# Optimization experiments

Hardware: AMD Instinct MI355X
Metric: run time of the kernel (lower is better)

## Reference

```python
import jax, jax.numpy as jnp
import numpy as np

PS = 2      # patch_size
TOPK = 3    # topk


def setup_inputs() -> dict:
    key = jax.random.key(0)
    x = jax.random.normal(key, (8, 128, 64, 64), dtype=jnp.float32)
    alpha = jnp.asarray(5.0, dtype=jnp.float32)  # nn.Parameter alpha
    return {"x": x, "alpha": alpha}


def _forward(x, alpha):
    ps = PS
    b, c, h, w = x.shape
    nph, npw = h // ps, w // ps
    npatch = nph * npw
    pa = ps * ps
    # F.normalize(p=2, dim=-3) with torch eps=1e-12
    norm = jnp.maximum(jnp.sqrt(jnp.sum(x * x, axis=1, keepdims=True)), 1e-12)
    x = x / norm
    # patchify -> [b, c, npatch, patch_area] (patches h-major, pixels row-major)
    xp = x.reshape(b, c, nph, ps, npw, ps).transpose(0, 1, 2, 4, 3, 5)
    xp = xp.reshape(b, c, npatch, pa)
    diag_idx = jnp.arange(ps) * (ps + 1)  # [0, 3] for ps=2
    # gather diagonal pixels of each patch -> [b, ps, npatch, c]
    xd = xp[:, :, :, diag_idx].transpose(0, 3, 2, 1)
    # patch correlation matmul -> [b, ps, npatch, npatch]
    corr = jnp.einsum('bpnc,bpmc->bpnm', xd, xd)
    avg = jnp.mean(corr, axis=1, keepdims=True)
    s = jnp.concatenate([corr, avg], axis=1)  # [b, ps+1, npatch, npatch]
    # ZeroWindow gaussian mask (rat_s=0.05); channel index = patch center (r,c)
    sr, sc = 0.05 * nph, 0.05 * npw
    rr = jnp.arange(nph, dtype=jnp.float32)
    cc = jnp.arange(npw, dtype=jnp.float32)
    cent_r, cent_c = jnp.meshgrid(rr, cc, indexing='ij')
    cent_r = cent_r.reshape(npatch)
    cent_c = cent_c.reshape(npatch)
    gr = jnp.exp(-(rr[None, :] - cent_r[:, None]) ** 2 / (2.0 * sr * sr))  # [npatch, nph]
    gc = jnp.exp(-(cc[None, :] - cent_c[:, None]) ** 2 / (2.0 * sc * sc))  # [npatch, npw]
    mask = (1.0 - gr[:, :, None] * gc[:, None, :]).reshape(npatch, npatch)
    s = s * mask[None, None]
    a = s * alpha
    # double (row + col) softmax
    s = jax.nn.softmax(a, axis=-1) * jax.nn.softmax(a, axis=-2)
    # expand avg channel to all patch pixels, scatter diagonal channels back
    new_x = jnp.broadcast_to(s[:, -1:], (b, pa, npatch, npatch))
    new_x = new_x.at[:, diag_idx].set(s[:, :ps])
    # un-patchify second npatch axis to spatial [b, npatch, h, w]
    y = jnp.swapaxes(new_x, 1, 3)  # [b, npatch, npatch, pa]
    y = y.reshape(b, npatch, nph, npw, ps, ps).transpose(0, 1, 2, 4, 3, 5)
    y = y.reshape(b, npatch, h, w)
    # topk over the npatch axis (dim=-3)
    vals = jax.lax.top_k(jnp.moveaxis(y, 1, -1), TOPK)[0]  # [b, h, w, k]
    return jnp.moveaxis(vals, -1, 1)  # [b, k, h, w]


def reference(x, alpha):
    return _forward(x, alpha)
```

## Files before the change

kernel.cpp:

```cpp
#include <hip/hip_runtime.h>
#include <hip/hip_bf16.h>
#include <math.h>

#define NB 8
#define NC 128
#define NH 64
#define NW 64
#define NP 1024
#define TWO_SIG2 5.12f

static const size_t RSUM_OFF_B = 0;
static const size_t PBUF_OFF_B = (size_t)NB * 3 * NP * 4;
static const size_t XD_OFF_B   = PBUF_OFF_B + (size_t)NB * NP * 3 * 4 * 3 * 4;

typedef __bf16 bf16x8 __attribute__((ext_vector_type(8)));
typedef float f32x4 __attribute__((ext_vector_type(4)));

__device__ __forceinline__ int iabs_(int v) { return v < 0 ? -v : v; }

#define INSERT3(v, A, Bq, Cq)                \
  {                                          \
    const float _c1 = fminf(A, (v));         \
    A = fmaxf(A, (v));                       \
    const float _c2 = fminf(Bq, _c1);        \
    Bq = fmaxf(Bq, _c1);                     \
    Cq = fmaxf(Cq, _c2);                     \
  }

#define MERGE3(a0, a1, a2, b0, b1, b2)       \
  {                                          \
    const float _x1 = fmaxf(a0, b0);         \
    const float _y1 = fminf(a0, b0);         \
    const float _x2 = fmaxf(a1, b1);         \
    const float _z  = fmaxf(a2, b2);         \
    a0 = _x1;                                \
    a1 = fmaxf(_y1, _x2);                    \
    a2 = fmaxf(fminf(_y1, _x2), _z);         \
  }

__global__ __launch_bounds__(256) void k1_norm(const float* __restrict__ x,
                                               __hip_bfloat16* __restrict__ xd) {
  __shared__ __align__(16) float tile[NC * 65];
  const int chunk = blockIdx.x;
  const int p = blockIdx.y;
  const int b = blockIdx.z;
  const int t = threadIdx.x;
  const int pix = t & 63;
  const int cw = t >> 6;
  const int nbase = chunk * 64;

  {
    const int n = nbase + pix;
    const int i = ((n >> 5) << 1) + p;
    const int j = ((n & 31) << 1) + p;
    const float* xb = x + (size_t)b * NC * NH * NW + (size_t)i * NW + j;
    for (int cc = 0; cc < 32; ++cc) {
      const int c = (cc << 2) + cw;
      tile[c * 65 + pix] = xb[(size_t)c * NH * NW];
    }
  }
  __syncthreads();

  const int lane = t & 63;
  const int w = t >> 6;
  for (int pg = 0; pg < 16; ++pg) {
    const int pixel = (pg << 2) + w;
    const float v0 = tile[lane * 65 + pixel];
    const float v1 = tile[(lane + 64) * 65 + pixel];
    float ss = v0 * v0 + v1 * v1;
#pragma unroll
    for (int m = 32; m >= 1; m >>= 1) ss += __shfl_xor(ss, m, 64);
    const float inv = 1.0f / fmaxf(sqrtf(ss), 1e-12f);
    __hip_bfloat16* xr = xd + ((size_t)((b * 2 + p) * NP) + nbase + pixel) * NC;
    xr[lane] = __float2bfloat16(v0 * inv);
    xr[lane + 64] = __float2bfloat16(v1 * inv);
  }
}

__global__ __launch_bounds__(256) void k2_sums(const ushort* __restrict__ xd,
                                               const float* __restrict__ alpha_p,
                                               float* __restrict__ rsum) {
  __shared__ __align__(16) __bf16 As[2][64 * 136];
  __shared__ __align__(16) __bf16 Bs[2][64 * 136];
  __shared__ float er[32];
  const int t = threadIdx.x;
  if (t < 32) er[t] = __expf(-(float)(t * t) / TWO_SIG2);

  const int cchunk = blockIdx.x;
  const int rowtile = blockIdx.y;
  const int b = blockIdx.z;
  const int i0 = rowtile << 6;
  const int jb = cchunk << 8;
  const float alpha = *alpha_p;

#pragma unroll
  for (int pl = 0; pl < 2; ++pl) {
    const float4* ga = (const float4*)(xd + ((size_t)(b * 2 + pl) * NP + i0) * NC);
#pragma unroll
    for (int it = 0; it < 4; ++it) {
      const int f = (it << 8) + t;
      const int r = f >> 4, q = f & 15;
      *(float4*)(&As[pl][r * 136 + q * 8]) = ga[f];
    }
  }

  const int wave = t >> 6;
  const int lane = t & 63;
  const int lrow = lane & 15;
  const int kq = lane >> 4;

  float sums[3][4];
#pragma unroll
  for (int ch = 0; ch < 3; ++ch)
#pragma unroll
    for (int reg = 0; reg < 4; ++reg) sums[ch][reg] = 0.f;

  for (int sc = 0; sc < 4; ++sc) {
    const int j0 = jb + (sc << 6);
    __syncthreads();
#pragma unroll
    for (int pl = 0; pl < 2; ++pl) {
      const float4* gb = (const float4*)(xd + ((size_t)(b * 2 + pl) * NP + j0) * NC);
#pragma unroll
      for (int it = 0; it < 4; ++it) {
        const int f = (it << 8) + t;
        const int r = f >> 4, q = f & 15;
        *(float4*)(&Bs[pl][r * 136 + q * 8]) = gb[f];
      }
    }
    __syncthreads();

    f32x4 acc[2][4];
#pragma unroll
    for (int pl = 0; pl < 2; ++pl)
#pragma unroll
      for (int ct = 0; ct < 4; ++ct)
#pragma unroll
        for (int u = 0; u < 4; ++u) acc[pl][ct][u] = 0.f;

#pragma unroll
    for (int kc = 0; kc < 4; ++kc) {
      const int kk = kc * 32 + (kq << 3);
      const bf16x8 a0 = *(const bf16x8*)(&As[0][(wave * 16 + lrow) * 136 + kk]);
      const bf16x8 a1 = *(const bf16x8*)(&As[1][(wave * 16 + lrow) * 136 + kk]);
#pragma unroll
      for (int ct = 0; ct < 4; ++ct) {
        const bf16x8 b0 = *(const bf16x8*)(&Bs[0][(ct * 16 + lrow) * 136 + kk]);
        const bf16x8 b1 = *(const bf16x8*)(&Bs[1][(ct * 16 + lrow) * 136 + kk]);
        acc[0][ct] = __builtin_amdgcn_mfma_f32_16x16x32_bf16(a0, b0, acc[0][ct], 0, 0, 0);
        acc[1][ct] = __builtin_amdgcn_mfma_f32_16x16x32_bf16(a1, b1, acc[1][ct], 0, 0, 0);
      }
    }

#pragma unroll
    for (int ct = 0; ct < 4; ++ct) {
      const int m = j0 + ct * 16 + lrow;
      const int rm = m >> 5, cm = m & 31;
#pragma unroll
      for (int reg = 0; reg < 4; ++reg) {
        const int n = i0 + wave * 16 + kq * 4 + reg;
        const int rn = n >> 5, cn = n & 31;
        const float g = er[iabs_(rn - rm)] * er[iabs_(cn - cm)];
        const float fm = alpha * (1.f - g);
        const float c0 = acc[0][ct][reg];
        const float c1 = acc[1][ct][reg];
        sums[0][reg] += __expf(fm * c0);
        sums[1][reg] += __expf(fm * c1);
        sums[2][reg] += __expf(fm * 0.5f * (c0 + c1));
      }
    }
  }

#pragma unroll
  for (int off = 1; off < 16; off <<= 1)
#pragma unroll
    for (int ch = 0; ch < 3; ++ch)
#pragma unroll
      for (int reg = 0; reg < 4; ++reg)
        sums[ch][reg] += __shfl_xor(sums[ch][reg], off, 64);

  if (lrow == 0) {
#pragma unroll
    for (int ch = 0; ch < 3; ++ch)
#pragma unroll
      for (int reg = 0; reg < 4; ++reg) {
        const int n = i0 + wave * 16 + kq * 4 + reg;
        atomicAdd(&rsum[((size_t)b * 3 + ch) * NP + n], sums[ch][reg]);
      }
  }
}

__global__ __launch_bounds__(256) void k4_topk(const ushort* __restrict__ xd,
                                               const float* __restrict__ alpha_p,
                                               const float* __restrict__ rsum,
                                               float* __restrict__ pbuf) {
  __shared__ __align__(16) __bf16 As[2][64 * 136];
  __shared__ __align__(16) __bf16 Bs[2][64 * 136];
  __shared__ float er[32];
  __shared__ float rsr[3][64];
  __shared__ float rsc[3][256];
  const int t = threadIdx.x;
  if (t < 32) er[t] = __expf(-(float)(t * t) / TWO_SIG2);

  const int cchunk = blockIdx.x;
  const int rowtile = blockIdx.y;
  const int b = blockIdx.z;
  const int i0 = rowtile << 6;
  const int jb = cchunk << 8;
  const float alpha = *alpha_p;

  if (t < 192) {
    const int ch = t >> 6, r = t & 63;
    rsr[ch][r] = 1.0f / rsum[((size_t)b * 3 + ch) * NP + i0 + r];
  }
#pragma unroll
  for (int ch = 0; ch < 3; ++ch)
    rsc[ch][t] = 1.0f / rsum[((size_t)b * 3 + ch) * NP + jb + t];

#pragma unroll
  for (int pl = 0; pl < 2; ++pl) {
    const float4* ga = (const float4*)(xd + ((size_t)(b * 2 + pl) * NP + i0) * NC);
#pragma unroll
    for (int it = 0; it < 4; ++it) {
      const int f = (it << 8) + t;
      const int r = f >> 4, q = f & 15;
      *(float4*)(&As[pl][r * 136 + q * 8]) = ga[f];
    }
  }

  const int wave = t >> 6;
  const int lane = t & 63;
  const int lrow = lane & 15;
  const int kq = lane >> 4;

  float tA[3][4], tB[3][4], tC[3][4];
#pragma unroll
  for (int ch = 0; ch < 3; ++ch)
#pragma unroll
    for (int reg = 0; reg < 4; ++reg) { tA[ch][reg] = -1e30f; tB[ch][reg] = -1e30f; tC[ch][reg] = -1e30f; }

  for (int sc = 0; sc < 4; ++sc) {
    const int j0 = jb + (sc << 6);
    __syncthreads();
#pragma unroll
    for (int pl = 0; pl < 2; ++pl) {
      const float4* gb = (const float4*)(xd + ((size_t)(b * 2 + pl) * NP + j0) * NC);
#pragma unroll
      for (int it = 0; it < 4; ++it) {
        const int f = (it << 8) + t;
        const int r = f >> 4, q = f & 15;
        *(float4*)(&Bs[pl][r * 136 + q * 8]) = gb[f];
      }
    }
    __syncthreads();

    f32x4 acc[2][4];
#pragma unroll
    for (int pl = 0; pl < 2; ++pl)
#pragma unroll
      for (int ct = 0; ct < 4; ++ct)
#pragma unroll
        for (int u = 0; u < 4; ++u) acc[pl][ct][u] = 0.f;

#pragma unroll
    for (int kc = 0; kc < 4; ++kc) {
      const int kk = kc * 32 + (kq << 3);
      const bf16x8 a0 = *(const bf16x8*)(&As[0][(wave * 16 + lrow) * 136 + kk]);
      const bf16x8 a1 = *(const bf16x8*)(&As[1][(wave * 16 + lrow) * 136 + kk]);
#pragma unroll
      for (int ct = 0; ct < 4; ++ct) {
        const bf16x8 b0 = *(const bf16x8*)(&Bs[0][(ct * 16 + lrow) * 136 + kk]);
        const bf16x8 b1 = *(const bf16x8*)(&Bs[1][(ct * 16 + lrow) * 136 + kk]);
        acc[0][ct] = __builtin_amdgcn_mfma_f32_16x16x32_bf16(a0, b0, acc[0][ct], 0, 0, 0);
        acc[1][ct] = __builtin_amdgcn_mfma_f32_16x16x32_bf16(a1, b1, acc[1][ct], 0, 0, 0);
      }
    }

#pragma unroll
    for (int ct = 0; ct < 4; ++ct) {
      const int mc = sc * 64 + ct * 16 + lrow;
      const int m = jb + mc;
      const int rm = m >> 5, cm = m & 31;
      const float im0 = rsc[0][mc], im1 = rsc[1][mc], im2 = rsc[2][mc];
#pragma unroll
      for (int reg = 0; reg < 4; ++reg) {
        const int nr = wave * 16 + kq * 4 + reg;
        const int n = i0 + nr;
        const int rn = n >> 5, cn = n & 31;
        const float g = er[iabs_(rn - rm)] * er[iabs_(cn - cm)];
        const float fm = alpha * (1.f - g);
        const float c0 = acc[0][ct][reg];
        const float c1 = acc[1][ct][reg];
        const float e0 = __expf(fm * c0);
        const float e1 = __expf(fm * c1);
        const float e2 = __expf(fm * 0.5f * (c0 + c1));
        const float q0 = e0 * e0 * rsr[0][nr] * im0;
        const float q1 = e1 * e1 * rsr[1][nr] * im1;
        const float q2 = e2 * e2 * rsr[2][nr] * im2;
        INSERT3(q0, tA[0][reg], tB[0][reg], tC[0][reg]);
        INSERT3(q1, tA[1][reg], tB[1][reg], tC[1][reg]);
        INSERT3(q2, tA[2][reg], tB[2][reg], tC[2][reg]);
      }
    }
  }

#pragma unroll
  for (int off = 1; off < 16; off <<= 1)
#pragma unroll
    for (int ch = 0; ch < 3; ++ch)
#pragma unroll
      for (int reg = 0; reg < 4; ++reg) {
        const float b0 = __shfl_xor(tA[ch][reg], off, 64);
        const float b1 = __shfl_xor(tB[ch][reg], off, 64);
        const float b2 = __shfl_xor(tC[ch][reg], off, 64);
        MERGE3(tA[ch][reg], tB[ch][reg], tC[ch][reg], b0, b1, b2);
      }

  if (lrow == 0) {
#pragma unroll
    for (int ch = 0; ch < 3; ++ch)
#pragma unroll
      for (int reg = 0; reg < 4; ++reg) {
        const int n = i0 + wave * 16 + kq * 4 + reg;
        const size_t base = ((((size_t)b * NP + n) * 3 + ch) * 4 + cchunk) * 3;
        pbuf[base + 0] = tA[ch][reg];
        pbuf[base + 1] = tB[ch][reg];
        pbuf[base + 2] = tC[ch][reg];
      }
  }
}

__global__ __launch_bounds__(256) void k5_merge(const float* __restrict__ pbuf,
                                                float* __restrict__ out) {
  const int tau = blockIdx.x * 256 + threadIdx.x;
  const int b = tau >> 10;
  const int n = tau & (NP - 1);
  const int rn = n >> 5, cn = n & 31;

  float f0[3], f1[3], f2[3];
#pragma unroll
  for (int ch = 0; ch < 3; ++ch) {
    const size_t base = (((size_t)tau * 3 + ch) * 4) * 3;
    f0[ch] = pbuf[base + 0];
    f1[ch] = pbuf[base + 1];
    f2[ch] = pbuf[base + 2];
#pragma unroll
    for (int p = 1; p < 4; ++p) {
      const float b0 = pbuf[base + p * 3 + 0];
      const float b1 = pbuf[base + p * 3 + 1];
      const float b2 = pbuf[base + p * 3 + 2];
      MERGE3(f0[ch], f1[ch], f2[ch], b0, b1, b2);
    }
  }

  float* ob = out + (size_t)b * 3 * (NH * NW);
  const int i00 = ((rn << 1) * NW) + (cn << 1);
#pragma unroll
  for (int tt = 0; tt < 3; ++tt) {
    float* op = ob + (size_t)tt * (NH * NW);
    const float r0 = (tt == 0) ? f0[0] : (tt == 1) ? f1[0] : f2[0];
    const float r1 = (tt == 0) ? f0[1] : (tt == 1) ? f1[1] : f2[1];
    const float r2 = (tt == 0) ? f0[2] : (tt == 1) ? f1[2] : f2[2];
    op[i00] = r0;
    op[i00 + NW + 1] = r1;
    op[i00 + 1] = r2;
    op[i00 + NW] = r2;
  }
}

extern "C" void kernel_launch(void* const* d_in, const int* in_sizes, int n_in,
                              void* d_out, int out_size, void* d_ws, size_t ws_size,
                              hipStream_t stream) {
  const float* x = (const float*)d_in[0];
  const float* alpha = (const float*)d_in[1];
  float* out = (float*)d_out;
  char* ws = (char*)d_ws;

  float* rsum = (float*)(ws + RSUM_OFF_B);
  float* pbuf = (float*)(ws + PBUF_OFF_B);
  __hip_bfloat16* xd = (__hip_bfloat16*)(ws + XD_OFF_B);

  hipMemsetAsync(rsum, 0, (size_t)NB * 3 * NP * sizeof(float), stream);
  k1_norm<<<dim3(16, 2, NB), 256, 0, stream>>>(x, xd);
  k2_sums<<<dim3(4, 16, NB), 256, 0, stream>>>((const ushort*)xd, alpha, rsum);
  k4_topk<<<dim3(4, 16, NB), 256, 0, stream>>>((const ushort*)xd, alpha, rsum, pbuf);
  k5_merge<<<dim3(32), 256, 0, stream>>>(pbuf, out);
}
```

Before: 119.1 us.

## Replace atomics with partial-sum buffer, fold alpha into exp2, med3 top-3 insert

The row-sum accumulation now writes per-column-chunk partial sums to a buffer, which removes the memset and the atomicAdds; the top-k kernel adds the four partials itself. The mask and alpha scaling are folded into one fma with a precomputed alpha*log2e table, and the exponential uses exp2f. The top-3 insert uses fmed3 with a zero initial value, since all candidates are non-negative. The row reciprocal is applied once at output instead of per element, and k1 loads float2 pairs. In exchange, the top-k kernel reads four partial sums per row and column, and the workspace layout changes.

Result: faster. 111.5 us (-6.4%).

```diff
diff --git a/kernel.cpp b/kernel.cpp
--- a/kernel.cpp
+++ b/kernel.cpp
@@ -8,9 +8,10 @@
 #define NW 64
 #define NP 1024
 #define TWO_SIG2 5.12f
-
-static const size_t RSUM_OFF_B = 0;
-static const size_t PBUF_OFF_B = (size_t)NB * 3 * NP * 4;
+#define LOG2E 1.44269504089f
+
+static const size_t PSUM_OFF_B = 0;
+static const size_t PBUF_OFF_B = (size_t)NB * 3 * 4 * NP * 4;
 static const size_t XD_OFF_B   = PBUF_OFF_B + (size_t)NB * NP * 3 * 4 * 3 * 4;
 
 typedef __bf16 bf16x8 __attribute__((ext_vector_type(8)));
@@ -18,13 +19,13 @@
 
 __device__ __forceinline__ int iabs_(int v) { return v < 0 ? -v : v; }
 
-#define INSERT3(v, A, Bq, Cq)                \
-  {                                          \
-    const float _c1 = fminf(A, (v));         \
-    A = fmaxf(A, (v));                       \
-    const float _c2 = fminf(Bq, _c1);        \
-    Bq = fmaxf(Bq, _c1);                     \
-    Cq = fmaxf(Cq, _c2);                     \
+#define INSERT3(v, A, Bq, Cq)                          \
+  {                                                    \
+    const float _na = fmaxf(A, (v));                   \
+    const float _nb = __builtin_amdgcn_fmed3f(A, Bq, (v)); \
+    Cq = __builtin_amdgcn_fmed3f(Bq, Cq, (v));         \
+    A = _na;                                           \
+    Bq = _nb;                                          \
   }
 
 #define MERGE3(a0, a1, a2, b0, b1, b2)       \
@@ -52,11 +53,12 @@
   {
     const int n = nbase + pix;
     const int i = ((n >> 5) << 1) + p;
-    const int j = ((n & 31) << 1) + p;
-    const float* xb = x + (size_t)b * NC * NH * NW + (size_t)i * NW + j;
+    const int jf = (n & 31);
+    const float* xb = x + (size_t)b * NC * NH * NW + (size_t)i * NW;
     for (int cc = 0; cc < 32; ++cc) {
       const int c = (cc << 2) + cw;
-      tile[c * 65 + pix] = xb[(size_t)c * NH * NW];
+      const float2 v2 = ((const float2*)(xb + (size_t)c * NH * NW))[jf];
+      tile[c * 65 + pix] = (p == 0) ? v2.x : v2.y;
     }
   }
   __syncthreads();
@@ -79,19 +81,24 @@
 
 __global__ __launch_bounds__(256) void k2_sums(const ushort* __restrict__ xd,
                                                const float* __restrict__ alpha_p,
-                                               float* __restrict__ rsum) {
+                                               float* __restrict__ psum) {
   __shared__ __align__(16) __bf16 As[2][64 * 136];
   __shared__ __align__(16) __bf16 Bs[2][64 * 136];
   __shared__ float er[32];
+  __shared__ float erA[32];
   const int t = threadIdx.x;
-  if (t < 32) er[t] = __expf(-(float)(t * t) / TWO_SIG2);
+  const float K = (*alpha_p) * LOG2E;
+  if (t < 32) {
+    const float e = __expf(-(float)(t * t) / TWO_SIG2);
+    er[t] = e;
+    erA[t] = K * e;
+  }
 
   const int cchunk = blockIdx.x;
   const int rowtile = blockIdx.y;
   const int b = blockIdx.z;
   const int i0 = rowtile << 6;
   const int jb = cchunk << 8;
-  const float alpha = *alpha_p;
 
 #pragma unroll
   for (int pl = 0; pl < 2; ++pl) {
@@ -160,13 +167,12 @@
       for (int reg = 0; reg < 4; ++reg) {
         const int n = i0 + wave * 16 + kq * 4 + reg;
         const int rn = n >> 5, cn = n & 31;
-        const float g = er[iabs_(rn - rm)] * er[iabs_(cn - cm)];
-        const float fm = alpha * (1.f - g);
-        const float c0 = acc[0][ct][reg];
-        const float c1 = acc[1][ct][reg];
-        sums[0][reg] += __expf(fm * c0);
-        sums[1][reg] += __expf(fm * c1);
-        sums[2][reg] += __expf(fm * 0.5f * (c0 + c1));
+        const float fm2 = fmaf(-erA[iabs_(rn - rm)], er[iabs_(cn - cm)], K);
+        const float g0 = fm2 * acc[0][ct][reg];
+        const float g1 = fm2 * acc[1][ct][reg];
+        sums[0][reg] += exp2f(g0);
+        sums[1][reg] += exp2f(g1);
+        sums[2][reg] += exp2f(0.5f * (g0 + g1));
       }
     }
   }
@@ -185,37 +191,45 @@
 #pragma unroll
       for (int reg = 0; reg < 4; ++reg) {
         const int n = i0 + wave * 16 + kq * 4 + reg;
-        atomicAdd(&rsum[((size_t)b * 3 + ch) * NP + n], sums[ch][reg]);
+        psum[(((size_t)b * 3 + ch) * 4 + cchunk) * NP + n] = sums[ch][reg];
       }
   }
 }
 
 __global__ __launch_bounds__(256) void k4_topk(const ushort* __restrict__ xd,
                                                const float* __restrict__ alpha_p,
-                                               const float* __restrict__ rsum,
+                                               const float* __restrict__ psum,
                                                float* __restrict__ pbuf) {
   __shared__ __align__(16) __bf16 As[2][64 * 136];
   __shared__ __align__(16) __bf16 Bs[2][64 * 136];
   __shared__ float er[32];
+  __shared__ float erA[32];
   __shared__ float rsr[3][64];
   __shared__ float rsc[3][256];
   const int t = threadIdx.x;
-  if (t < 32) er[t] = __expf(-(float)(t * t) / TWO_SIG2);
+  const float K = (*alpha_p) * LOG2E;
+  if (t < 32) {
+    const float e = __expf(-(float)(t * t) / TWO_SIG2);
+    er[t] = e;
+    erA[t] = K * e;
+  }
 
   const int cchunk = blockIdx.x;
   const int rowtile = blockIdx.y;
   const int b = blockIdx.z;
   const int i0 = rowtile << 6;
   const int jb = cchunk << 8;
-  const float alpha = *alpha_p;
 
   if (t < 192) {
     const int ch = t >> 6, r = t & 63;
-    rsr[ch][r] = 1.0f / rsum[((size_t)b * 3 + ch) * NP + i0 + r];
-  }
-#pragma unroll
-  for (int ch = 0; ch < 3; ++ch)
-    rsc[ch][t] = 1.0f / rsum[((size_t)b * 3 + ch) * NP + jb + t];
+    const float* pp = psum + ((size_t)b * 3 + ch) * 4 * NP + i0 + r;
+    rsr[ch][r] = 1.0f / (pp[0] + pp[NP] + pp[2 * NP] + pp[3 * NP]);
+  }
+#pragma unroll
+  for (int ch = 0; ch < 3; ++ch) {
+    const float* pp = psum + ((size_t)b * 3 + ch) * 4 * NP + jb + t;
+    rsc[ch][t] = 1.0f / (pp[0] + pp[NP] + pp[2 * NP] + pp[3 * NP]);
+  }
 
 #pragma unroll
   for (int pl = 0; pl < 2; ++pl) {
@@ -237,7 +251,7 @@
 #pragma unroll
   for (int ch = 0; ch < 3; ++ch)
 #pragma unroll
-    for (int reg = 0; reg < 4; ++reg) { tA[ch][reg] = -1e30f; tB[ch][reg] = -1e30f; tC[ch][reg] = -1e30f; }
+    for (int reg = 0; reg < 4; ++reg) { tA[ch][reg] = 0.f; tB[ch][reg] = 0.f; tC[ch][reg] = 0.f; }
 
   for (int sc = 0; sc < 4; ++sc) {
     const int j0 = jb + (sc << 6);
@@ -287,16 +301,15 @@
         const int nr = wave * 16 + kq * 4 + reg;
         const int n = i0 + nr;
         const int rn = n >> 5, cn = n & 31;
-        const float g = er[iabs_(rn - rm)] * er[iabs_(cn - cm)];
-        const float fm = alpha * (1.f - g);
-        const float c0 = acc[0][ct][reg];
-        const float c1 = acc[1][ct][reg];
-        const float e0 = __expf(fm * c0);
-        const float e1 = __expf(fm * c1);
-        const float e2 = __expf(fm * 0.5f * (c0 + c1));
-        const float q0 = e0 * e0 * rsr[0][nr] * im0;
-        const float q1 = e1 * e1 * rsr[1][nr] * im1;
-        const float q2 = e2 * e2 * rsr[2][nr] * im2;
+        const float fm2 = fmaf(-erA[iabs_(rn - rm)], er[iabs_(cn - cm)], K);
+        const float g0 = fm2 * acc[0][ct][reg];
+        const float g1 = fm2 * acc[1][ct][reg];
+        const float e0 = exp2f(g0);
+        const float e1 = exp2f(g1);
+        const float e2 = exp2f(0.5f * (g0 + g1));
+        const float q0 = e0 * e0 * im0;
+        const float q1 = e1 * e1 * im1;
+        const float q2 = e2 * e2 * im2;
         INSERT3(q0, tA[0][reg], tB[0][reg], tC[0][reg]);
         INSERT3(q1, tA[1][reg], tB[1][reg], tC[1][reg]);
         INSERT3(q2, tA[2][reg], tB[2][reg], tC[2][reg]);
@@ -321,11 +334,13 @@
     for (int ch = 0; ch < 3; ++ch)
 #pragma unroll
       for (int reg = 0; reg < 4; ++reg) {
-        const int n = i0 + wave * 16 + kq * 4 + reg;
+        const int nr = wave * 16 + kq * 4 + reg;
+        const int n = i0 + nr;
+        const float irn = rsr[ch][nr];
         const size_t base = ((((size_t)b * NP + n) * 3 + ch) * 4 + cchunk) * 3;
-        pbuf[base + 0] = tA[ch][reg];
-        pbuf[base + 1] = tB[ch][reg];
-        pbuf[base + 2] = tC[ch][reg];
+        pbuf[base + 0] = tA[ch][reg] * irn;
+        pbuf[base + 1] = tB[ch][reg] * irn;
+        pbuf[base + 2] = tC[ch][reg] * irn;
       }
   }
 }
@@ -376,13 +391,12 @@
   float* out = (float*)d_out;
   char* ws = (char*)d_ws;
 
-  float* rsum = (float*)(ws + RSUM_OFF_B);
+  float* psum = (float*)(ws + PSUM_OFF_B);
   float* pbuf = (float*)(ws + PBUF_OFF_B);
   __hip_bfloat16* xd = (__hip_bfloat16*)(ws + XD_OFF_B);
 
-  hipMemsetAsync(rsum, 0, (size_t)NB * 3 * NP * sizeof(float), stream);
   k1_norm<<<dim3(16, 2, NB), 256, 0, stream>>>(x, xd);
-  k2_sums<<<dim3(4, 16, NB), 256, 0, stream>>>((const ushort*)xd, alpha, rsum);
-  k4_topk<<<dim3(4, 16, NB), 256, 0, stream>>>((const ushort*)xd, alpha, rsum, pbuf);
+  k2_sums<<<dim3(4, 16, NB), 256, 0, stream>>>((const ushort*)xd, alpha, psum);
+  k4_topk<<<dim3(4, 16, NB), 256, 0, stream>>>((const ushort*)xd, alpha, psum, pbuf);
   k5_merge<<<dim3(32), 256, 0, stream>>>(pbuf, out);
 }
```
